# Performance work log

Hardware: AMD Instinct MI355X
Metric: run time of the kernel (lower is better)

## Reference

```python
import jax, jax.numpy as jnp
import numpy as np

IMG, P, CIN, D, NH, NB, NC = 512, 16, 3, 384, 4, 3, 2
HD = D // NH
NP_ = (IMG // P) ** 2
T = NP_ + 1
FF = 4 * D


def _ln(x, s, b, eps=1e-5):
    m = x.mean(-1, keepdims=True)
    v = ((x - m) ** 2).mean(-1, keepdims=True)
    return (x - m) / jnp.sqrt(v + eps) * s + b


def setup_inputs() -> dict:
    key = jax.random.key(0)
    ks = jax.random.split(key, 20)
    s = 0.02
    inp = {
        'x': jax.random.normal(ks[0], (16, CIN, IMG, IMG), jnp.float32),
        'targets': jax.random.randint(ks[1], (16,), 0, NC),
        'conv_w': jax.random.normal(ks[2], (D, CIN, P, P), jnp.float32) * s,
        'conv_b': jnp.zeros((D,), jnp.float32),
        'cls_token': jax.random.normal(ks[3], (1, 1, D), jnp.float32),
        'pos_emb': jax.random.normal(ks[4], (T, D), jnp.float32) * s,
        'ln1_s': jnp.ones((NB, D), jnp.float32), 'ln1_b': jnp.zeros((NB, D), jnp.float32),
        'ln2_s': jnp.ones((NB, D), jnp.float32), 'ln2_b': jnp.zeros((NB, D), jnp.float32),
        'wq': jax.random.normal(ks[5], (NB, D, D), jnp.float32) * s,
        'wk': jax.random.normal(ks[6], (NB, D, D), jnp.float32) * s,
        'wv': jax.random.normal(ks[7], (NB, D, D), jnp.float32) * s,
        'wo': jax.random.normal(ks[8], (NB, D, D), jnp.float32) * s,
        'bo': jnp.zeros((NB, D), jnp.float32),
        'w1': jax.random.normal(ks[9], (NB, D, FF), jnp.float32) * s,
        'b1': jnp.zeros((NB, FF), jnp.float32),
        'w2': jax.random.normal(ks[10], (NB, FF, D), jnp.float32) * s,
        'b2': jnp.zeros((NB, D), jnp.float32),
        'lnf_s': jnp.ones((D,), jnp.float32), 'lnf_b': jnp.zeros((D,), jnp.float32),
        'proj_w': jax.random.normal(ks[11], (D, NC), jnp.float32) * s,
        'proj_b': jnp.zeros((NC,), jnp.float32),
    }
    return inp


def _forward(x, conv_w, conv_b, cls_token, pos_emb, ln1_s, ln1_b, ln2_s, ln2_b,
             wq, wk, wv, wo, bo, w1, b1, w2, b2, lnf_s, lnf_b, proj_w, proj_b):
    B = x.shape[0]
    # patch embedding: conv with kernel==stride == non-overlapping patches
    xp = x.reshape(B, CIN, IMG // P, P, IMG // P, P)
    pe = jnp.einsum('bchpwq,dcpq->bhwd', xp, conv_w).reshape(B, NP_, D) + conv_b
    h = jnp.concatenate([jnp.broadcast_to(cls_token, (B, 1, D)), pe], axis=1)  # (B,T,D)
    h = h + pos_emb
    scale = HD ** (-0.5)
    for i in range(NB):
        hn = _ln(h, ln1_s[i], ln1_b[i])
        q = (hn @ wq[i]).reshape(B, T, NH, HD).transpose(0, 2, 1, 3)
        k = (hn @ wk[i]).reshape(B, T, NH, HD).transpose(0, 2, 1, 3)
        v = (hn @ wv[i]).reshape(B, T, NH, HD).transpose(0, 2, 1, 3)
        # cdist p=2 (Euclidean distance) attention scores
        d2 = (jnp.sum(q * q, -1)[..., :, None] + jnp.sum(k * k, -1)[..., None, :]
              - 2.0 * jnp.einsum('bhqd,bhkd->bhqk', q, k))
        wei = jax.nn.softmax(jnp.sqrt(jnp.maximum(d2, 0.0)) * scale, axis=-1)
        vals = jnp.einsum('bhqk,bhkd->bhqd', wei, v).transpose(0, 2, 1, 3).reshape(B, T, D)
        h = h + vals @ wo[i] + bo[i]
        hn2 = _ln(h, ln2_s[i], ln2_b[i])
        h = h + jax.nn.relu(hn2 @ w1[i] + b1[i]) @ w2[i] + b2[i]
    h = _ln(h, lnf_s, lnf_b)
    logits = h @ proj_w + proj_b
    return logits[:, 0]  # (B, NC) cls-token logits


def reference(x, targets, conv_w, conv_b, cls_token, pos_emb, ln1_s, ln1_b, ln2_s, ln2_b,
              wq, wk, wv, wo, bo, w1, b1, w2, b2, lnf_s, lnf_b, proj_w, proj_b):
    cls_logits = _forward(x, conv_w, conv_b, cls_token, pos_emb, ln1_s, ln1_b, ln2_s, ln2_b,
                          wq, wk, wv, wo, bo, w1, b1, w2, b2, lnf_s, lnf_b, proj_w, proj_b)
    logp = jax.nn.log_softmax(cls_logits, axis=-1)
    loss = -jnp.mean(jnp.take_along_axis(logp, targets[:, None], axis=1))
    return (cls_logits, loss)
```

## Files before the change

### kernel.cpp

```cpp
#include <hip/hip_runtime.h>
#include <math.h>


#define BATCH   16
#define TSEQ    1025
#define DMODEL  384
#define NHEAD   4
#define HDIM    96
#define NBLK    3
#define FFDIM   1536
#define IMGSZ   512
#define NPATCHI 1024
#define MROWS   (BATCH*TSEQ)
#define MPATCH  (BATCH*NPATCHI)
#define KPE     768
#define VTS     1088
#define SKS     1088
#define ATT_SCALE 0.10206207261596577f

typedef __attribute__((ext_vector_type(8))) __bf16 bf16x8;
typedef __attribute__((ext_vector_type(4))) __bf16 bf16x4;
typedef __attribute__((ext_vector_type(4))) float  f32x4;
typedef unsigned int u32;

__device__ __forceinline__ f32x4 fzero4() {
  f32x4 v; v[0] = 0.f; v[1] = 0.f; v[2] = 0.f; v[3] = 0.f; return v;
}
__device__ __forceinline__ bf16x8 bzero8() {
  bf16x8 v;
#pragma unroll
  for (int j = 0; j < 8; ++j) v[j] = (__bf16)0.f;
  return v;
}

__device__ __forceinline__ void gl_lds16(const __bf16* g, __bf16* l) {
  __builtin_amdgcn_global_load_lds(
      (const __attribute__((address_space(1))) u32*)g,
      (__attribute__((address_space(3))) u32*)l, 16, 0, 0);
}

template<int EPI>
__global__ __launch_bounds__(256, 4) void mgemm_k(
    const __bf16* __restrict__ A, const __bf16* __restrict__ Bt,
    const float* __restrict__ bias, const float* __restrict__ res,
    float* __restrict__ Cf, __bf16* __restrict__ Cb, int M, int N, int K)
{
  __shared__ __bf16 Al[2][128][32];
  __shared__ __bf16 Bl[2][128][32];
  const int tid = threadIdx.x;
  const int lane = tid & 63;
  const int w = tid >> 6;
  const int wr = w >> 1, wc = w & 1;
  const int l15 = lane & 15, g = lane >> 4;
  const int row0 = blockIdx.x * 128, col0 = blockIdx.y * 128;
  const int sr = w * 32 + (lane >> 2);
  const int sc = (lane & 3) * 8;
  const __bf16* Ab = A  + (size_t)(row0 + sr) * K + sc;
  const __bf16* Bb = Bt + (size_t)(col0 + sr) * K + sc;

  f32x4 acc[4][4];
#pragma unroll
  for (int i = 0; i < 4; ++i)
#pragma unroll
    for (int j = 0; j < 4; ++j) acc[i][j] = fzero4();

  const int nk = K >> 5;
  auto stage = [&](int buf, int kt) {
#pragma unroll
    for (int j = 0; j < 2; ++j) {
      gl_lds16(Ab + (size_t)(j * 16) * K + kt * 32, &Al[buf][w * 32 + j * 16][0]);
      gl_lds16(Bb + (size_t)(j * 16) * K + kt * 32, &Bl[buf][w * 32 + j * 16][0]);
    }
  };

  stage(0, 0);
  __syncthreads();
  int cur = 0;
  for (int kt = 0; kt < nk; ++kt) {
    if (kt + 1 < nk) stage(cur ^ 1, kt + 1);
    bf16x8 af[4], bfr[4];
#pragma unroll
    for (int mi = 0; mi < 4; ++mi)
      af[mi] = *(const bf16x8*)&Al[cur][wr * 64 + mi * 16 + l15][g * 8];
#pragma unroll
    for (int ni = 0; ni < 4; ++ni)
      bfr[ni] = *(const bf16x8*)&Bl[cur][wc * 64 + ni * 16 + l15][g * 8];
    __builtin_amdgcn_s_setprio(1);
#pragma unroll
    for (int mi = 0; mi < 4; ++mi)
#pragma unroll
      for (int ni = 0; ni < 4; ++ni)
        acc[mi][ni] = __builtin_amdgcn_mfma_f32_16x16x32_bf16(
            af[mi], bfr[ni], acc[mi][ni], 0, 0, 0);
    __builtin_amdgcn_s_setprio(0);
    __syncthreads();
    cur ^= 1;
  }
#pragma unroll
  for (int ni = 0; ni < 4; ++ni) {
    const int gc = col0 + wc * 64 + ni * 16 + l15;
    const float bv = (EPI & 1) ? bias[gc] : 0.f;
#pragma unroll
    for (int mi = 0; mi < 4; ++mi) {
#pragma unroll
      for (int r = 0; r < 4; ++r) {
        const int gr = row0 + wr * 64 + mi * 16 + g * 4 + r;
        if (gr >= M) continue;
        float v = acc[mi][ni][r] + bv;
        if (EPI & 2) v = fmaxf(v, 0.f);
        if (EPI & 4) v += res[(size_t)gr * N + gc];
        if (EPI & 8)  Cf[(size_t)gr * N + gc] = v;
        if (EPI & 16) Cb[(size_t)gr * N + gc] = (__bf16)v;
      }
    }
  }
}

__global__ void vtr_k(const __bf16* __restrict__ qkv, __bf16* __restrict__ Vt)
{
  __shared__ __bf16 t[32][33];
  const int bh = blockIdx.z;
  const int bb = bh >> 2, hh = bh & 3;
  const int t0 = blockIdx.x * 32;
  const int d0 = blockIdx.y * 32;
  const int tx = threadIdx.x, ty = threadIdx.y;
#pragma unroll
  for (int i = 0; i < 4; ++i) {
    const int tt = t0 + ty + 8 * i;
    t[ty + 8 * i][tx] = (tt < TSEQ)
        ? qkv[(size_t)(bb * TSEQ + tt) * 1152 + 768 + hh * 96 + d0 + tx]
        : (__bf16)0.f;
  }
  __syncthreads();
#pragma unroll
  for (int i = 0; i < 4; ++i)
    Vt[((size_t)bh * 96 + d0 + ty + 8 * i) * VTS + t0 + tx] = t[tx][ty + 8 * i];
}

__global__ __launch_bounds__(256, 2) void attn_k(
    const __bf16* __restrict__ qkv, const __bf16* __restrict__ Vtg,
    const float* __restrict__ sq2, const float* __restrict__ sk2,
    __bf16* __restrict__ O)
{
  __shared__ __bf16 Kl[2][64][104];
  __shared__ __bf16 Vl[2][96][72];
  __shared__ __bf16 Pl[4][32][72];
  const int bid = blockIdx.x;
  const int xcd = bid & 7, jj = bid >> 3;
  const int j9 = jj / 9;
  const int bh = xcd * 8 + j9;
  const int qt = jj - j9 * 9;
  const int bb = bh >> 2, hh = bh & 3;
  const int tid = threadIdx.x;
  const int w = tid >> 6, lane = tid & 63;
  const int l15 = lane & 15, g = lane >> 4;
  const int q0 = qt * 128 + w * 32;
  const float* sq2h = sq2 + (size_t)bh * SKS;
  const float* sk2h = sk2 + (size_t)bh * SKS;
  const __bf16* vbase = Vtg + (size_t)bh * 96 * VTS;

  bf16x8 qf[2][3];
  float sqv[2];
#pragma unroll
  for (int m = 0; m < 2; ++m) {
    int qr = q0 + m * 16 + l15; if (qr > TSEQ - 1) qr = TSEQ - 1;
    const __bf16* qp = qkv + (size_t)(bb * TSEQ + qr) * 1152 + hh * 96 + g * 8;
#pragma unroll
    for (int kf = 0; kf < 3; ++kf) qf[m][kf] = *(const bf16x8*)(qp + kf * 32);
    sqv[m] = sq2h[qr];
  }

  float mrun[2] = {-INFINITY, -INFINITY};
  float lrun[2] = {0.f, 0.f};
  f32x4 accO[2][6];
#pragma unroll
  for (int m = 0; m < 2; ++m)
#pragma unroll
    for (int n = 0; n < 6; ++n) accO[m][n] = fzero4();

  bf16x8 kr[3], vr[3];
  auto load_chunk = [&](int c) {
    const int kbase = c * 64;
#pragma unroll
    for (int i = 0; i < 3; ++i) {
      const int idx = tid + i * 256;
      const int row = idx / 12, cc = idx - row * 12;
      const int kg = kbase + row;
      kr[i] = (kg < TSEQ)
          ? *(const bf16x8*)(qkv + (size_t)(bb * TSEQ + kg) * 1152 + 384
                             + hh * 96 + cc * 8)
          : bzero8();
      const int d = idx >> 3, o8 = (idx & 7) * 8;
      vr[i] = *(const bf16x8*)(vbase + (size_t)d * VTS + kbase + o8);
    }
  };

  load_chunk(0);
  int cur = 0;
  for (int c = 0; c < 17; ++c) {
    const int kbase = c * 64;
#pragma unroll
    for (int i = 0; i < 3; ++i) {
      const int idx = tid + i * 256;
      const int row = idx / 12, cc = idx - row * 12;
      *(bf16x8*)&Kl[cur][row][cc * 8] = kr[i];
      const int d = idx >> 3, o8 = (idx & 7) * 8;
      *(bf16x8*)&Vl[cur][d][o8] = vr[i];
    }
    __syncthreads();
    if (c < 16) load_chunk(c + 1);

    f32x4 sfT[2][4];
#pragma unroll
    for (int m = 0; m < 2; ++m)
#pragma unroll
      for (int ks = 0; ks < 4; ++ks) sfT[m][ks] = fzero4();
    __builtin_amdgcn_s_setprio(1);
#pragma unroll
    for (int ks = 0; ks < 4; ++ks) {
      bf16x8 kb0 = *(const bf16x8*)&Kl[cur][ks * 16 + l15][g * 8];
      bf16x8 kb1 = *(const bf16x8*)&Kl[cur][ks * 16 + l15][32 + g * 8];
      bf16x8 kb2 = *(const bf16x8*)&Kl[cur][ks * 16 + l15][64 + g * 8];
#pragma unroll
      for (int m = 0; m < 2; ++m) {
        sfT[m][ks] = __builtin_amdgcn_mfma_f32_16x16x32_bf16(kb0, qf[m][0], sfT[m][ks], 0, 0, 0);
        sfT[m][ks] = __builtin_amdgcn_mfma_f32_16x16x32_bf16(kb1, qf[m][1], sfT[m][ks], 0, 0, 0);
        sfT[m][ks] = __builtin_amdgcn_mfma_f32_16x16x32_bf16(kb2, qf[m][2], sfT[m][ks], 0, 0, 0);
      }
    }
    __builtin_amdgcn_s_setprio(0);

    float cm[2] = {-INFINITY, -INFINITY};
#pragma unroll
    for (int ks = 0; ks < 4; ++ks) {
      const int sb = kbase + ks * 16 + g * 4;
      const float4 skv = *(const float4*)&sk2h[sb];
      const float sk4[4] = {skv.x, skv.y, skv.z, skv.w};
#pragma unroll
      for (int m = 0; m < 2; ++m)
#pragma unroll
        for (int r = 0; r < 4; ++r) {
          const float d2 = sqv[m] + sk4[r] - 2.f * sfT[m][ks][r];
          const float s = (sb + r < TSEQ)
              ? sqrtf(fmaxf(d2, 0.f)) * ATT_SCALE : -INFINITY;
          sfT[m][ks][r] = s;
          cm[m] = fmaxf(cm[m], s);
        }
    }

    const int ok = (cm[0] <= mrun[0] + 8.f) && (cm[1] <= mrun[1] + 8.f);
    if (!__all(ok)) {
#pragma unroll
      for (int m = 0; m < 2; ++m) {
        float v = cm[m];
        v = fmaxf(v, __shfl_xor(v, 16, 64));
        v = fmaxf(v, __shfl_xor(v, 32, 64));
        const float mn = fmaxf(mrun[m], v);
        const float f = __expf(mrun[m] - mn);
        mrun[m] = mn;
        lrun[m] *= f;
#pragma unroll
        for (int r = 0; r < 4; ++r) {
          const float fb = __shfl(f, g * 4 + r, 64);
#pragma unroll
          for (int n = 0; n < 6; ++n) accO[m][n][r] *= fb;
        }
      }
    }

#pragma unroll
    for (int m = 0; m < 2; ++m) {
      float psum = 0.f;
#pragma unroll
      for (int ks = 0; ks < 4; ++ks) {
        bf16x4 pw;
#pragma unroll
        for (int r = 0; r < 4; ++r) {
          const float p = __expf(sfT[m][ks][r] - mrun[m]);
          psum += p;
          pw[r] = (__bf16)p;
        }
        *(bf16x4*)&Pl[w][m * 16 + l15][ks * 16 + g * 4] = pw;
      }
      psum += __shfl_xor(psum, 16, 64);
      psum += __shfl_xor(psum, 32, 64);
      lrun[m] += psum;
    }

    __builtin_amdgcn_s_setprio(1);
#pragma unroll
    for (int ks2 = 0; ks2 < 2; ++ks2) {
      bf16x8 pa[2];
#pragma unroll
      for (int m = 0; m < 2; ++m)
        pa[m] = *(const bf16x8*)&Pl[w][m * 16 + l15][ks2 * 32 + g * 8];
#pragma unroll
      for (int n = 0; n < 6; ++n) {
        bf16x8 vb = *(const bf16x8*)&Vl[cur][n * 16 + l15][ks2 * 32 + g * 8];
#pragma unroll
        for (int m = 0; m < 2; ++m)
          accO[m][n] = __builtin_amdgcn_mfma_f32_16x16x32_bf16(pa[m], vb, accO[m][n], 0, 0, 0);
      }
    }
    __builtin_amdgcn_s_setprio(0);
    cur ^= 1;
  }

#pragma unroll
  for (int m = 0; m < 2; ++m)
#pragma unroll
    for (int r = 0; r < 4; ++r) {
      const int qr = q0 + m * 16 + g * 4 + r;
      if (qr >= TSEQ) continue;
      const float lv = __shfl(lrun[m], g * 4 + r, 64);
      const float inv = 1.f / lv;
#pragma unroll
      for (int n = 0; n < 6; ++n)
        O[(size_t)(bb * TSEQ + qr) * 384 + hh * 96 + n * 16 + l15] =
            (__bf16)(accO[m][n][r] * inv);
    }
}

__global__ __launch_bounds__(256) void im2col_k(
    const float* __restrict__ x, __bf16* __restrict__ Ai)
{
  const int i = blockIdx.x * 256 + threadIdx.x;
  const int row = i / 96;
  const int k = (i - row * 96) * 8;
  const int b = row >> 10;
  const int pidx = row & 1023;
  const int py = pidx >> 5, px = pidx & 31;
  const int cc = k >> 8;
  const int rem = k & 255;
  const int p = rem >> 4, q = rem & 15;
  const float* src = x + ((size_t)((b * 3 + cc) * IMGSZ + py * 16 + p)) * IMGSZ
                       + px * 16 + q;
  const float4 a = *(const float4*)src;
  const float4 c4 = *(const float4*)(src + 4);
  bf16x8 o;
  o[0] = (__bf16)a.x;  o[1] = (__bf16)a.y;  o[2] = (__bf16)a.z;  o[3] = (__bf16)a.w;
  o[4] = (__bf16)c4.x; o[5] = (__bf16)c4.y; o[6] = (__bf16)c4.z; o[7] = (__bf16)c4.w;
  *(bf16x8*)&Ai[(size_t)i * 8] = o;
}

__global__ void wt_k(const float* __restrict__ src, size_t srcZ,
                     __bf16* __restrict__ dst, size_t dstZ, int K, int N)
{
  __shared__ float t[32][33];
  const float* s = src + blockIdx.z * srcZ;
  __bf16* d = dst + blockIdx.z * dstZ;
  const int k0 = blockIdx.x * 32, n0 = blockIdx.y * 32;
  const int tx = threadIdx.x, ty = threadIdx.y;
#pragma unroll
  for (int i = 0; i < 4; ++i)
    t[ty + 8 * i][tx] = s[(size_t)(k0 + ty + 8 * i) * N + n0 + tx];
  __syncthreads();
#pragma unroll
  for (int i = 0; i < 4; ++i)
    d[(size_t)(n0 + ty + 8 * i) * K + k0 + tx] = (__bf16)t[tx][ty + 8 * i];
}

__global__ void cvt_k(const float* __restrict__ src, __bf16* __restrict__ dst, int n8)
{
  const int i = blockIdx.x * 256 + threadIdx.x;
  if (i >= n8) return;
  const float4 a = *(const float4*)&src[(size_t)i * 8];
  const float4 b = *(const float4*)&src[(size_t)i * 8 + 4];
  bf16x8 o;
  o[0] = (__bf16)a.x; o[1] = (__bf16)a.y; o[2] = (__bf16)a.z; o[3] = (__bf16)a.w;
  o[4] = (__bf16)b.x; o[5] = (__bf16)b.y; o[6] = (__bf16)b.z; o[7] = (__bf16)b.w;
  *(bf16x8*)&dst[(size_t)i * 8] = o;
}

__global__ __launch_bounds__(256) void embed_k(
    const float* __restrict__ pe, const float* __restrict__ cls,
    const float* __restrict__ pos, float* __restrict__ h)
{
  const int i = blockIdx.x * 256 + threadIdx.x;
  const int row = i / 96;
  const int d4 = (i - row * 96) * 4;
  const int b = row / TSEQ;
  const int t = row - b * TSEQ;
  const float4 po = *(const float4*)&pos[(size_t)t * DMODEL + d4];
  float4 r;
  if (t == 0) {
    const float4 cv = *(const float4*)&cls[d4];
    r = make_float4(cv.x + po.x, cv.y + po.y, cv.z + po.z, cv.w + po.w);
  } else {
    const float4 pv = *(const float4*)&pe[((size_t)(b * NPATCHI + t - 1)) * DMODEL + d4];
    r = make_float4(pv.x + po.x, pv.y + po.y, pv.z + po.z, pv.w + po.w);
  }
  *(float4*)&h[(size_t)row * DMODEL + d4] = r;
}

__global__ __launch_bounds__(256) void ln_k(
    const float* __restrict__ in, const float* __restrict__ sc,
    const float* __restrict__ bi, __bf16* __restrict__ out)
{
  const int w = threadIdx.x >> 6, lane = threadIdx.x & 63;
  const int row = blockIdx.x * 4 + w;
  const float* r = in + (size_t)row * DMODEL;
  float v[6], sum = 0.f, ss = 0.f;
#pragma unroll
  for (int j = 0; j < 6; ++j) {
    const float xv = r[lane + 64 * j];
    v[j] = xv; sum += xv; ss += xv * xv;
  }
#pragma unroll
  for (int m = 1; m < 64; m <<= 1) {
    sum += __shfl_xor(sum, m, 64);
    ss  += __shfl_xor(ss,  m, 64);
  }
  const float mean = sum * (1.f / 384.f);
  const float var  = ss * (1.f / 384.f) - mean * mean;
  const float rstd = rsqrtf(var + 1e-5f);
  __bf16* o = out + (size_t)row * DMODEL;
#pragma unroll
  for (int j = 0; j < 6; ++j) {
    const int col = lane + 64 * j;
    o[col] = (__bf16)((v[j] - mean) * rstd * sc[col] + bi[col]);
  }
}

__global__ __launch_bounds__(256) void sumsq_k(
    const __bf16* __restrict__ qkv, float* __restrict__ sq2,
    float* __restrict__ sk2)
{
  const int w = threadIdx.x >> 6, lane = threadIdx.x & 63;
  const int row = blockIdx.x * 4 + w;
  const int h = lane >> 4, lg = lane & 15;
  const __bf16* q = qkv + (size_t)row * 1152 + h * HDIM;
  float s1 = 0.f, s2 = 0.f;
#pragma unroll
  for (int j = 0; j < 6; ++j) {
    const float a = (float)q[lg + 16 * j];
    const float c = (float)q[384 + lg + 16 * j];
    s1 += a * a; s2 += c * c;
  }
#pragma unroll
  for (int m = 1; m < 16; m <<= 1) {
    s1 += __shfl_xor(s1, m, 64);
    s2 += __shfl_xor(s2, m, 64);
  }
  if (lg == 0) {
    const int b = row / TSEQ, t = row - b * TSEQ;
    sq2[((size_t)b * NHEAD + h) * SKS + t] = s1;
    sk2[((size_t)b * NHEAD + h) * SKS + t] = s2;
  }
}

__global__ __launch_bounds__(256) void head_k(
    const float* __restrict__ h, const float* __restrict__ gs,
    const float* __restrict__ gb, const float* __restrict__ pw,
    const float* __restrict__ pb, const int* __restrict__ tgt,
    float* __restrict__ out)
{
  __shared__ float lg[BATCH][2];
  const int w = threadIdx.x >> 6, lane = threadIdx.x & 63;
  for (int b = w; b < BATCH; b += 4) {
    const float* r = h + (size_t)b * TSEQ * DMODEL;
    float v[6], sum = 0.f, ss = 0.f;
#pragma unroll
    for (int j = 0; j < 6; ++j) {
      const float xv = r[lane + 64 * j];
      v[j] = xv; sum += xv; ss += xv * xv;
    }
#pragma unroll
    for (int m = 1; m < 64; m <<= 1) {
      sum += __shfl_xor(sum, m, 64);
      ss  += __shfl_xor(ss,  m, 64);
    }
    const float mean = sum * (1.f / 384.f);
    const float var  = ss * (1.f / 384.f) - mean * mean;
    const float rstd = rsqrtf(var + 1e-5f);
    float l0 = 0.f, l1 = 0.f;
#pragma unroll
    for (int j = 0; j < 6; ++j) {
      const int col = lane + 64 * j;
      const float hnv = (v[j] - mean) * rstd * gs[col] + gb[col];
      l0 = fmaf(hnv, pw[col * 2 + 0], l0);
      l1 = fmaf(hnv, pw[col * 2 + 1], l1);
    }
#pragma unroll
    for (int m = 1; m < 64; m <<= 1) {
      l0 += __shfl_xor(l0, m, 64);
      l1 += __shfl_xor(l1, m, 64);
    }
    if (lane == 0) { lg[b][0] = l0 + pb[0]; lg[b][1] = l1 + pb[1]; }
  }
  __syncthreads();
  if (threadIdx.x < 32)
    out[threadIdx.x] = lg[threadIdx.x >> 1][threadIdx.x & 1];
  if (threadIdx.x == 0) {
    float acc = 0.f;
    for (int b = 0; b < BATCH; ++b) {
      const float a = lg[b][0], c = lg[b][1];
      const float mx = fmaxf(a, c);
      const float lse = mx + logf(expf(a - mx) + expf(c - mx));
      const float lp = ((tgt[b] == 0) ? a : c) - lse;
      acc += lp;
    }
    out[32] = -acc * (1.f / BATCH);
  }
}

extern "C" void kernel_launch(void* const* d_in, const int* in_sizes, int n_in,
                              void* d_out, int out_size, void* d_ws, size_t ws_size,
                              hipStream_t stream)
{
  const float* x       = (const float*)d_in[0];
  const int*   targets = (const int*)  d_in[1];
  const float* conv_w  = (const float*)d_in[2];
  const float* conv_b  = (const float*)d_in[3];
  const float* cls_tok = (const float*)d_in[4];
  const float* pos_emb = (const float*)d_in[5];
  const float* ln1_s   = (const float*)d_in[6];
  const float* ln1_b   = (const float*)d_in[7];
  const float* ln2_s   = (const float*)d_in[8];
  const float* ln2_b   = (const float*)d_in[9];
  const float* wq      = (const float*)d_in[10];
  const float* wk      = (const float*)d_in[11];
  const float* wv      = (const float*)d_in[12];
  const float* wo      = (const float*)d_in[13];
  const float* bo      = (const float*)d_in[14];
  const float* w1      = (const float*)d_in[15];
  const float* b1      = (const float*)d_in[16];
  const float* w2      = (const float*)d_in[17];
  const float* b2      = (const float*)d_in[18];
  const float* lnf_s   = (const float*)d_in[19];
  const float* lnf_b   = (const float*)d_in[20];
  const float* proj_w  = (const float*)d_in[21];
  const float* proj_b  = (const float*)d_in[22];

  char* p = (char*)d_ws;
  auto alloc = [&](size_t bytes) -> void* {
    void* r = (void*)p; p += (bytes + 255) & ~(size_t)255; return r;
  };
  float*  h     = (float*) alloc((size_t)MROWS * DMODEL * 4);
  __bf16* hn    = (__bf16*)alloc((size_t)MROWS * DMODEL * 2);
  __bf16* qkv   = (__bf16*)alloc((size_t)MROWS * 1152 * 2);
  __bf16* Obuf  = (__bf16*)alloc((size_t)MROWS * DMODEL * 2);
  float*  pe    = (float*) alloc((size_t)MPATCH * DMODEL * 4);
  float*  sq2   = (float*) alloc((size_t)BATCH * NHEAD * SKS * 4);
  float*  sk2   = (float*) alloc((size_t)BATCH * NHEAD * SKS * 4);
  __bf16* cwb   = (__bf16*)alloc((size_t)DMODEL * KPE * 2);
  __bf16* wqkvT = (__bf16*)alloc((size_t)NBLK * 1152 * DMODEL * 2);
  __bf16* woT   = (__bf16*)alloc((size_t)NBLK * DMODEL * DMODEL * 2);
  __bf16* w1T   = (__bf16*)alloc((size_t)NBLK * FFDIM * DMODEL * 2);
  __bf16* w2T   = (__bf16*)alloc((size_t)NBLK * DMODEL * FFDIM * 2);
  if ((size_t)(p - (char*)d_ws) > ws_size) return;
  __bf16* Ai  = qkv;
  __bf16* ffb = qkv;
  __bf16* Vtg = (__bf16*)pe;

  cvt_k<<<144, 256, 0, stream>>>(conv_w, cwb, (DMODEL * KPE) / 8);
  {
    dim3 blk(32, 8);
    wt_k<<<dim3(12, 12, 3), blk, 0, stream>>>(wq, (size_t)DMODEL * DMODEL,
        wqkvT + 0,               (size_t)1152 * DMODEL, DMODEL, DMODEL);
    wt_k<<<dim3(12, 12, 3), blk, 0, stream>>>(wk, (size_t)DMODEL * DMODEL,
        wqkvT + 384 * DMODEL,    (size_t)1152 * DMODEL, DMODEL, DMODEL);
    wt_k<<<dim3(12, 12, 3), blk, 0, stream>>>(wv, (size_t)DMODEL * DMODEL,
        wqkvT + 768 * DMODEL,    (size_t)1152 * DMODEL, DMODEL, DMODEL);
    wt_k<<<dim3(12, 12, 3), blk, 0, stream>>>(wo, (size_t)DMODEL * DMODEL,
        woT, (size_t)DMODEL * DMODEL, DMODEL, DMODEL);
    wt_k<<<dim3(12, 48, 3), blk, 0, stream>>>(w1, (size_t)DMODEL * FFDIM,
        w1T, (size_t)FFDIM * DMODEL, DMODEL, FFDIM);
    wt_k<<<dim3(48, 12, 3), blk, 0, stream>>>(w2, (size_t)FFDIM * DMODEL,
        w2T, (size_t)DMODEL * FFDIM, FFDIM, DMODEL);
  }

  im2col_k<<<6144, 256, 0, stream>>>(x, Ai);
  mgemm_k<9><<<dim3(128, 3), 256, 0, stream>>>(
      Ai, cwb, conv_b, nullptr, pe, nullptr, MPATCH, DMODEL, KPE);
  embed_k<<<6150, 256, 0, stream>>>(pe, cls_tok, pos_emb, h);

  for (int i = 0; i < NBLK; ++i) {
    ln_k<<<4100, 256, 0, stream>>>(h, ln1_s + i * DMODEL, ln1_b + i * DMODEL, hn);
    mgemm_k<16><<<dim3(129, 9), 256, 0, stream>>>(
        hn, wqkvT + (size_t)i * 1152 * DMODEL, nullptr, nullptr,
        nullptr, qkv, MROWS, 1152, DMODEL);
    sumsq_k<<<4100, 256, 0, stream>>>(qkv, sq2, sk2);
    vtr_k<<<dim3(34, 3, 64), dim3(32, 8), 0, stream>>>(qkv, Vtg);
    attn_k<<<576, 256, 0, stream>>>(qkv, Vtg, sq2, sk2, Obuf);
    mgemm_k<13><<<dim3(129, 3), 256, 0, stream>>>(
        Obuf, woT + (size_t)i * DMODEL * DMODEL, bo + i * DMODEL, h,
        h, nullptr, MROWS, DMODEL, DMODEL);
    ln_k<<<4100, 256, 0, stream>>>(h, ln2_s + i * DMODEL, ln2_b + i * DMODEL, hn);
    mgemm_k<19><<<dim3(129, 12), 256, 0, stream>>>(
        hn, w1T + (size_t)i * FFDIM * DMODEL, b1 + i * FFDIM, nullptr,
        nullptr, ffb, MROWS, FFDIM, DMODEL);
    mgemm_k<13><<<dim3(129, 3), 256, 0, stream>>>(
        ffb, w2T + (size_t)i * DMODEL * FFDIM, b2 + i * DMODEL, h,
        h, nullptr, MROWS, DMODEL, FFDIM);
  }

  head_k<<<1, 256, 0, stream>>>(h, lnf_s, lnf_b, proj_w, proj_b, targets,
                                (float*)d_out);
}
```

Before: 1.143 ms.

## Triple-buffer GEMM with LDS swizzle and fold attention scale into exp2 domain

The GEMM moves from double to triple buffering with a prefetch distance of two, using explicit vmcnt waits and barriers, and applies an XOR swizzle to LDS columns to cut bank conflicts. The launch-bounds occupancy hint drops from 4 to 3 blocks to fit the larger LDS footprint. The attention kernel folds scale², the -2 factor and log2(e) into precomputed norms and an FMA, so sqrt directly yields log2-domain scores and exp2f replaces __expf. It also adds a fast path without tail masking for full key tiles. The lazy-rescale threshold is adjusted to match the log2 domain.

```diff
diff --git a/kernel.cpp b/kernel.cpp
--- a/kernel.cpp
+++ b/kernel.cpp
@@ -16,7 +16,9 @@
 #define KPE     768
 #define VTS     1088
 #define SKS     1088
-#define ATT_SCALE 0.10206207261596577f
+#define C2SC    0.0216809269f
+#define N2C2    (-0.0433618538f)
+#define THR2    11.5416f
 
 typedef __attribute__((ext_vector_type(8))) __bf16 bf16x8;
 typedef __attribute__((ext_vector_type(4))) __bf16 bf16x4;
@@ -40,13 +42,13 @@
 }
 
 template<int EPI>
-__global__ __launch_bounds__(256, 4) void mgemm_k(
+__global__ __launch_bounds__(256, 3) void mgemm_k(
     const __bf16* __restrict__ A, const __bf16* __restrict__ Bt,
     const float* __restrict__ bias, const float* __restrict__ res,
     float* __restrict__ Cf, __bf16* __restrict__ Cb, int M, int N, int K)
 {
-  __shared__ __bf16 Al[2][128][32];
-  __shared__ __bf16 Bl[2][128][32];
+  __shared__ __bf16 Al[3][128][32];
+  __shared__ __bf16 Bl[3][128][32];
   const int tid = threadIdx.x;
   const int lane = tid & 63;
   const int w = tid >> 6;
@@ -54,9 +56,10 @@
   const int l15 = lane & 15, g = lane >> 4;
   const int row0 = blockIdx.x * 128, col0 = blockIdx.y * 128;
   const int sr = w * 32 + (lane >> 2);
-  const int sc = (lane & 3) * 8;
+  const int sc = ((lane & 3) ^ ((lane >> 3) & 3)) * 8;
   const __bf16* Ab = A  + (size_t)(row0 + sr) * K + sc;
   const __bf16* Bb = Bt + (size_t)(col0 + sr) * K + sc;
+  const int rcol = (g ^ ((l15 >> 1) & 3)) * 8;
 
   f32x4 acc[4][4];
 #pragma unroll
@@ -74,17 +77,20 @@
   };
 
   stage(0, 0);
-  __syncthreads();
-  int cur = 0;
+  stage(1, 1);
+  asm volatile("s_waitcnt vmcnt(4)" ::: "memory");
+  __builtin_amdgcn_s_barrier();
+
+  int cur = 0, pre = 2;
   for (int kt = 0; kt < nk; ++kt) {
-    if (kt + 1 < nk) stage(cur ^ 1, kt + 1);
+    if (kt + 2 < nk) stage(pre, kt + 2);
     bf16x8 af[4], bfr[4];
 #pragma unroll
     for (int mi = 0; mi < 4; ++mi)
-      af[mi] = *(const bf16x8*)&Al[cur][wr * 64 + mi * 16 + l15][g * 8];
+      af[mi] = *(const bf16x8*)&Al[cur][wr * 64 + mi * 16 + l15][rcol];
 #pragma unroll
     for (int ni = 0; ni < 4; ++ni)
-      bfr[ni] = *(const bf16x8*)&Bl[cur][wc * 64 + ni * 16 + l15][g * 8];
+      bfr[ni] = *(const bf16x8*)&Bl[cur][wc * 64 + ni * 16 + l15][rcol];
     __builtin_amdgcn_s_setprio(1);
 #pragma unroll
     for (int mi = 0; mi < 4; ++mi)
@@ -93,9 +99,17 @@
         acc[mi][ni] = __builtin_amdgcn_mfma_f32_16x16x32_bf16(
             af[mi], bfr[ni], acc[mi][ni], 0, 0, 0);
     __builtin_amdgcn_s_setprio(0);
-    __syncthreads();
-    cur ^= 1;
-  }
+    if (kt + 2 < nk) {
+      asm volatile("s_waitcnt vmcnt(4)" ::: "memory");
+      __builtin_amdgcn_s_barrier();
+    } else if (kt + 1 < nk) {
+      asm volatile("s_waitcnt vmcnt(0)" ::: "memory");
+      __builtin_amdgcn_s_barrier();
+    }
+    pre = cur;
+    cur = (cur == 2) ? 0 : cur + 1;
+  }
+
 #pragma unroll
   for (int ni = 0; ni < 4; ++ni) {
     const int gc = col0 + wc * 64 + ni * 16 + l15;
@@ -231,24 +245,41 @@
     __builtin_amdgcn_s_setprio(0);
 
     float cm[2] = {-INFINITY, -INFINITY};
-#pragma unroll
-    for (int ks = 0; ks < 4; ++ks) {
-      const int sb = kbase + ks * 16 + g * 4;
-      const float4 skv = *(const float4*)&sk2h[sb];
-      const float sk4[4] = {skv.x, skv.y, skv.z, skv.w};
-#pragma unroll
-      for (int m = 0; m < 2; ++m)
-#pragma unroll
-        for (int r = 0; r < 4; ++r) {
-          const float d2 = sqv[m] + sk4[r] - 2.f * sfT[m][ks][r];
-          const float s = (sb + r < TSEQ)
-              ? sqrtf(fmaxf(d2, 0.f)) * ATT_SCALE : -INFINITY;
-          sfT[m][ks][r] = s;
-          cm[m] = fmaxf(cm[m], s);
+    if (kbase + 64 <= TSEQ) {
+#pragma unroll
+      for (int ks = 0; ks < 4; ++ks) {
+        const int sb2 = kbase + ks * 16 + g * 4;
+        const float4 skv = *(const float4*)&sk2h[sb2];
+#pragma unroll
+        for (int m = 0; m < 2; ++m) {
+          const float t0 = sqrtf(fmaxf(fmaf(sfT[m][ks][0], N2C2, sqv[m] + skv.x), 0.f));
+          const float t1 = sqrtf(fmaxf(fmaf(sfT[m][ks][1], N2C2, sqv[m] + skv.y), 0.f));
+          const float t2 = sqrtf(fmaxf(fmaf(sfT[m][ks][2], N2C2, sqv[m] + skv.z), 0.f));
+          const float t3 = sqrtf(fmaxf(fmaf(sfT[m][ks][3], N2C2, sqv[m] + skv.w), 0.f));
+          sfT[m][ks][0] = t0; sfT[m][ks][1] = t1;
+          sfT[m][ks][2] = t2; sfT[m][ks][3] = t3;
+          cm[m] = fmaxf(fmaxf(fmaxf(cm[m], t0), fmaxf(t1, t2)), t3);
         }
-    }
-
-    const int ok = (cm[0] <= mrun[0] + 8.f) && (cm[1] <= mrun[1] + 8.f);
+      }
+    } else {
+#pragma unroll
+      for (int ks = 0; ks < 4; ++ks) {
+        const int sb2 = kbase + ks * 16 + g * 4;
+        const float4 skv = *(const float4*)&sk2h[sb2];
+        const float sk4[4] = {skv.x, skv.y, skv.z, skv.w};
+#pragma unroll
+        for (int m = 0; m < 2; ++m)
+#pragma unroll
+          for (int r = 0; r < 4; ++r) {
+            float t = sqrtf(fmaxf(fmaf(sfT[m][ks][r], N2C2, sqv[m] + sk4[r]), 0.f));
+            t = (sb2 + r < TSEQ) ? t : -INFINITY;
+            sfT[m][ks][r] = t;
+            cm[m] = fmaxf(cm[m], t);
+          }
+      }
+    }
+
+    const int ok = (cm[0] <= mrun[0] + THR2) && (cm[1] <= mrun[1] + THR2);
     if (!__all(ok)) {
 #pragma unroll
       for (int m = 0; m < 2; ++m) {
@@ -256,7 +287,7 @@
         v = fmaxf(v, __shfl_xor(v, 16, 64));
         v = fmaxf(v, __shfl_xor(v, 32, 64));
         const float mn = fmaxf(mrun[m], v);
-        const float f = __expf(mrun[m] - mn);
+        const float f = exp2f(mrun[m] - mn);
         mrun[m] = mn;
         lrun[m] *= f;
 #pragma unroll
@@ -276,7 +307,7 @@
         bf16x4 pw;
 #pragma unroll
         for (int r = 0; r < 4; ++r) {
-          const float p = __expf(sfT[m][ks][r] - mrun[m]);
+          const float p = exp2f(sfT[m][ks][r] - mrun[m]);
           psum += p;
           pw[r] = (__bf16)p;
         }
@@ -444,8 +475,8 @@
   }
   if (lg == 0) {
     const int b = row / TSEQ, t = row - b * TSEQ;
-    sq2[((size_t)b * NHEAD + h) * SKS + t] = s1;
-    sk2[((size_t)b * NHEAD + h) * SKS + t] = s2;
+    sq2[((size_t)b * NHEAD + h) * SKS + t] = s1 * C2SC;
+    sk2[((size_t)b * NHEAD + h) * SKS + t] = s2 * C2SC;
   }
 }
 
```

Result: slower. 1.191 ms (+4.2%).
